# Optimization experiments

Measured on AMD Instinct MI355X. Metric: run time of the kernel, lower is better.

Reference implementation:

```python
import jax, jax.numpy as jnp
import numpy as np

N_NODES = 100000
N_EDGES = 1600000
S_FEAT = 16   # static node features
D_FEAT = 8    # dynamic node features
E_FEAT = 4    # edge features
K = 2
EDGE_IN = E_FEAT + 2 * S_FEAT + 2 * D_FEAT  # 52
HIDDEN = 2 * D_FEAT                          # 16


def setup_inputs() -> dict:
    key = jax.random.key(0)
    ks = jax.random.split(key, 12)
    inp = {
        "x_s": jax.random.normal(ks[0], (N_NODES, S_FEAT), jnp.float32),
        "x_d": jax.random.normal(ks[1], (N_NODES, D_FEAT), jnp.float32),
        "edge_attr": jax.random.normal(ks[2], (N_EDGES, E_FEAT), jnp.float32),
        # edge MLP: Linear(EDGE_IN->HIDDEN) + ReLU + Linear(HIDDEN->D_FEAT)
        "W1": jax.random.normal(ks[3], (HIDDEN, EDGE_IN), jnp.float32) / np.sqrt(EDGE_IN),
        "b1": jnp.zeros((HIDDEN,), jnp.float32),
        "W2": jax.random.normal(ks[4], (D_FEAT, HIDDEN), jnp.float32) / np.sqrt(HIDDEN),
        "b2": jnp.zeros((D_FEAT,), jnp.float32),
        # K+1 = 3 filter matrices, Linear(D->D, bias=False): y = x @ W.T
        "Wf0": jax.random.normal(ks[5], (D_FEAT, D_FEAT), jnp.float32) / np.sqrt(D_FEAT),
        "Wf1": jax.random.normal(ks[6], (D_FEAT, D_FEAT), jnp.float32) / np.sqrt(D_FEAT),
        "Wf2": jax.random.normal(ks[7], (D_FEAT, D_FEAT), jnp.float32) / np.sqrt(D_FEAT),
        "edge_index": jax.random.randint(ks[8], (2, N_EDGES), 0, N_NODES, jnp.int64
                                         if jax.config.jax_enable_x64 else jnp.int32),
    }
    return inp


def _edge_mlp(e, W1, b1, W2, b2):
    h = jax.nn.relu(e @ W1.T + b1)
    return h @ W2.T + b2


def reference(x_s, x_d, edge_attr, W1, b1, W2, b2, Wf0, Wf1, Wf2, edge_index):
    row, col = edge_index[0], edge_index[1]
    num_nodes = x_d.shape[0]

    # s_ij depends only on static inputs (x_s, x_d, edge_attr), not on `out`,
    # so it is identical across the K steps; compute it once. The per-step
    # boolean edge mask is applied multiplicatively below, which matches the
    # torch masked-gather/scatter exactly (normalization is per-edge).
    e_ij = jnp.concatenate(
        [x_s[row], x_s[col], x_d[row], x_d[col], edge_attr], axis=1)  # [E, 52]
    s_ij = _edge_mlp(e_ij, W1, b1, W2, b2)                            # [E, D]
    nrm = jnp.linalg.norm(s_ij, axis=1, keepdims=True)
    s_ij = jnp.where(nrm > 0, s_ij / jnp.where(nrm > 0, nrm, 1.0), 0.0)

    filters = [Wf0, Wf1, Wf2]
    out = x_d @ filters[0].T
    for k in range(K):
        mask = out.sum(1) != 0                         # [N]
        edge_mask = (mask[row] | mask[col]).astype(out.dtype)  # [E]
        hydraulic_gradient = out[col] - out[row]       # [E, D]
        shift_sum = hydraulic_gradient * s_ij * edge_mask[:, None]
        scattered = jax.ops.segment_sum(shift_sum, col, num_segments=num_nodes)
        scattered = scattered @ filters[k + 1].T
        out = out + scattered
    return out
```

## Files before the change

### kernel.cpp

```cpp
#include <hip/hip_runtime.h>
#include <hip/hip_fp16.h>

#define S_FEAT 16
#define D_FEAT 8
#define E_FEAT 4
#define EDGE_IN 52
#define HIDDEN 16
#define SCAN_CHUNK 2048
#define NSUB 8

typedef unsigned int uint4v __attribute__((ext_vector_type(4)));
typedef float float4v __attribute__((ext_vector_type(4)));
typedef int int2v __attribute__((ext_vector_type(2)));

__device__ __forceinline__ void mlp_sij(
    const float* __restrict__ x_s, const float* __restrict__ x_d,
    const float* __restrict__ edge_attr,
    const float* __restrict__ W1, const float* __restrict__ b1,
    const float* __restrict__ W2, const float* __restrict__ b2,
    int row, int col, int e, float s[D_FEAT])
{
    float in[EDGE_IN];
    {
        const float4* p = (const float4*)(x_s + (size_t)row * S_FEAT);
#pragma unroll
        for (int q = 0; q < 4; ++q) {
            float4 v = p[q];
            in[q * 4 + 0] = v.x; in[q * 4 + 1] = v.y;
            in[q * 4 + 2] = v.z; in[q * 4 + 3] = v.w;
        }
    }
    {
        const float4* p = (const float4*)(x_s + (size_t)col * S_FEAT);
#pragma unroll
        for (int q = 0; q < 4; ++q) {
            float4 v = p[q];
            in[16 + q * 4 + 0] = v.x; in[16 + q * 4 + 1] = v.y;
            in[16 + q * 4 + 2] = v.z; in[16 + q * 4 + 3] = v.w;
        }
    }
    {
        const float4* p = (const float4*)(x_d + (size_t)row * D_FEAT);
#pragma unroll
        for (int q = 0; q < 2; ++q) {
            float4 v = p[q];
            in[32 + q * 4 + 0] = v.x; in[32 + q * 4 + 1] = v.y;
            in[32 + q * 4 + 2] = v.z; in[32 + q * 4 + 3] = v.w;
        }
    }
    {
        const float4* p = (const float4*)(x_d + (size_t)col * D_FEAT);
#pragma unroll
        for (int q = 0; q < 2; ++q) {
            float4 v = p[q];
            in[40 + q * 4 + 0] = v.x; in[40 + q * 4 + 1] = v.y;
            in[40 + q * 4 + 2] = v.z; in[40 + q * 4 + 3] = v.w;
        }
    }
    {
        float4 v = *(const float4*)(edge_attr + (size_t)e * E_FEAT);
        in[48] = v.x; in[49] = v.y; in[50] = v.z; in[51] = v.w;
    }

    float h[HIDDEN];
#pragma unroll
    for (int i = 0; i < HIDDEN; ++i) {
        float acc = b1[i];
#pragma unroll
        for (int j = 0; j < EDGE_IN; ++j)
            acc = fmaf(in[j], W1[i * EDGE_IN + j], acc);
        h[i] = acc > 0.f ? acc : 0.f;
    }

    float nrm2 = 0.f;
#pragma unroll
    for (int i = 0; i < D_FEAT; ++i) {
        float acc = b2[i];
#pragma unroll
        for (int j = 0; j < HIDDEN; ++j)
            acc = fmaf(h[j], W2[i * HIDDEN + j], acc);
        s[i] = acc;
        nrm2 = fmaf(acc, acc, nrm2);
    }
    float nrm = sqrtf(nrm2);
    float inv = nrm > 0.f ? 1.f / nrm : 0.f;
#pragma unroll
    for (int i = 0; i < D_FEAT; ++i) s[i] *= inv;
}

__device__ __forceinline__ uint4v pack_rec(const float s[8], int row)
{
    int q[8];
#pragma unroll
    for (int i = 0; i < 8; ++i) {
        float v = fminf(fmaxf(s[i] * 2047.f, -2047.f), 2047.f);
        q[i] = (int)rintf(v) & 0xFFF;
    }
    uint4v r;
    r[0] = (unsigned)(q[0] | (q[1] << 12) | (q[2] << 24));
    r[1] = (unsigned)((q[2] >> 8) | (q[3] << 4) | (q[4] << 16) | (q[5] << 28));
    r[2] = (unsigned)((q[5] >> 4) | (q[6] << 8) | (q[7] << 20));
    r[3] = (unsigned)row;
    return r;
}

__device__ __forceinline__ float rec_s(uint4v r, int f)
{
    int off = f * 12;
    unsigned lo = off < 32 ? r[0] : (off < 64 ? r[1] : r[2]);
    unsigned hi = off < 32 ? r[1] : (off < 64 ? r[2] : 0u);
    unsigned sh = (unsigned)off & 31u;
    unsigned long long both = ((unsigned long long)hi << 32) | lo;
    int q = ((int)((unsigned)(both >> sh) << 20)) >> 20;
    return (float)q * (1.f / 2047.f);
}

__device__ __forceinline__ void unpack8h(uint4v w, float* dst)
{
#pragma unroll
    for (int i = 0; i < 4; ++i) {
        unsigned u = w[i];
        __half2 h = *reinterpret_cast<__half2*>(&u);
        float2 f = __half22float2(h);
        dst[2 * i] = f.x; dst[2 * i + 1] = f.y;
    }
}

__global__ __launch_bounds__(256) void zero_counts_kernel(int* __restrict__ counts, int M)
{
    int i = blockIdx.x * blockDim.x + threadIdx.x;
    if (i < M) counts[i] = 0;
}

__global__ __launch_bounds__(256) void hist_kernel(
    const int* __restrict__ ei, int E, int N, int* __restrict__ counts8)
{
    int e = blockIdx.x * blockDim.x + threadIdx.x;
    if (e >= E) return;
    int col = __builtin_nontemporal_load(ei + E + e);
    atomicAdd(&counts8[(threadIdx.x & (NSUB - 1)) * N + col], 1);
}

__global__ __launch_bounds__(256) void scan_local_kernel(
    const int* __restrict__ counts8, int* __restrict__ partial,
    int* __restrict__ blocksums, int N)
{
    __shared__ int sh[256];
    int b = blockIdx.x, t = threadIdx.x;
    int base = b * SCAN_CHUNK + t * 8;
    int v[8];
    int run = 0;
#pragma unroll
    for (int j = 0; j < 8; ++j) {
        int c = 0;
        if (base + j < N) {
#pragma unroll
            for (int s8 = 0; s8 < NSUB; ++s8)
                c += counts8[s8 * N + base + j];
        }
        v[j] = run;
        run += c;
    }
    sh[t] = run;
    __syncthreads();
#pragma unroll
    for (int st = 1; st < 256; st <<= 1) {
        int x = (t >= st) ? sh[t - st] : 0;
        __syncthreads();
        sh[t] += x;
        __syncthreads();
    }
    int excl = sh[t] - run;
    if (t == 255) blocksums[b] = sh[255];
#pragma unroll
    for (int j = 0; j < 8; ++j)
        if (base + j < N) partial[base + j] = excl + v[j];
}

__global__ __launch_bounds__(64) void scan_blk_kernel(int* __restrict__ bs, int NB)
{
    int lane = threadIdx.x;
    int carry = 0;
    for (int base = 0; base < NB; base += 64) {
        int i = base + lane;
        int orig = (i < NB) ? bs[i] : 0;
        int v = orig;
#pragma unroll
        for (int st = 1; st < 64; st <<= 1) {
            int t = __shfl_up(v, st);
            if (lane >= st) v += t;
        }
        if (i < NB) bs[i] = carry + v - orig;
        carry += __shfl(v, 63);
    }
}

__global__ __launch_bounds__(256) void scan_add_kernel(
    int* __restrict__ offsets, int* __restrict__ cursor,
    const int* __restrict__ blocksums, int N, int E)
{
    int i = blockIdx.x * blockDim.x + threadIdx.x;
    if (i < N) {
        int off = offsets[i] + blocksums[i / SCAN_CHUNK];
        offsets[i] = off;
        cursor[i]  = off;
    } else if (i == N) {
        offsets[N] = E;
    }
}

__global__ __launch_bounds__(256) void proj_scan_kernel(
    int* __restrict__ offsets, int* __restrict__ cursor,
    const int* __restrict__ blocksums,
    const float* __restrict__ x_s, const float* __restrict__ x_d,
    const float* __restrict__ W1, const float* __restrict__ b1,
    const float* __restrict__ Wf0,
    __half* __restrict__ PRh, __half* __restrict__ PCh,
    float* __restrict__ out, int N, int E)
{
    int n = blockIdx.x * blockDim.x + threadIdx.x;
    if (n > N) return;
    if (n == N) { offsets[N] = E; return; }
    {
        int off = offsets[n] + blocksums[n / SCAN_CHUNK];
        offsets[n] = off;
        cursor[n]  = off;
    }
    float xs[S_FEAT], xd[D_FEAT];
    {
        const float4* p = (const float4*)(x_s + (size_t)n * S_FEAT);
#pragma unroll
        for (int q = 0; q < 4; ++q) {
            float4 v = p[q];
            xs[q * 4 + 0] = v.x; xs[q * 4 + 1] = v.y;
            xs[q * 4 + 2] = v.z; xs[q * 4 + 3] = v.w;
        }
        const float4* pd = (const float4*)(x_d + (size_t)n * D_FEAT);
        float4 a = pd[0], b = pd[1];
        xd[0] = a.x; xd[1] = a.y; xd[2] = a.z; xd[3] = a.w;
        xd[4] = b.x; xd[5] = b.y; xd[6] = b.z; xd[7] = b.w;
    }
    __half prh[HIDDEN], pch[HIDDEN];
#pragma unroll
    for (int i = 0; i < HIDDEN; ++i) {
        const float* w = W1 + i * EDGE_IN;
        float a = b1[i], c = 0.f;
#pragma unroll
        for (int j = 0; j < S_FEAT; ++j) {
            a = fmaf(xs[j], w[j], a);
            c = fmaf(xs[j], w[16 + j], c);
        }
#pragma unroll
        for (int j = 0; j < D_FEAT; ++j) {
            a = fmaf(xd[j], w[32 + j], a);
            c = fmaf(xd[j], w[40 + j], c);
        }
        prh[i] = __float2half_rn(a);
        pch[i] = __float2half_rn(c);
    }
    {
        uint4v* pr = (uint4v*)(PRh + (size_t)n * HIDDEN);
        uint4v* pc = (uint4v*)(PCh + (size_t)n * HIDDEN);
        pr[0] = *(uint4v*)&prh[0]; pr[1] = *(uint4v*)&prh[8];
        pc[0] = *(uint4v*)&pch[0]; pc[1] = *(uint4v*)&pch[8];
    }
    float o[D_FEAT];
#pragma unroll
    for (int i = 0; i < D_FEAT; ++i) {
        float acc = 0.f;
#pragma unroll
        for (int j = 0; j < D_FEAT; ++j)
            acc = fmaf(xd[j], Wf0[i * D_FEAT + j], acc);
        o[i] = acc;
    }
    float4* op = (float4*)(out + (size_t)n * D_FEAT);
    op[0] = make_float4(o[0], o[1], o[2], o[3]);
    op[1] = make_float4(o[4], o[5], o[6], o[7]);
}

__device__ __forceinline__ void edge_work(
    const __half* __restrict__ PRh, const __half* __restrict__ PCh,
    const float* __restrict__ edge_attr,
    const float* __restrict__ W1,
    const float* __restrict__ W2, const float* __restrict__ b2,
    int row, int col, int e,
    int* __restrict__ cursor, uint4v* __restrict__ recs)
{
    float pr[HIDDEN], pc[HIDDEN];
    {
        const uint4v* p = (const uint4v*)(PRh + (size_t)row * HIDDEN);
        const uint4v* c = (const uint4v*)(PCh + (size_t)col * HIDDEN);
        uint4v p0 = p[0], p1 = p[1], c0 = c[0], c1 = c[1];
        unpack8h(p0, pr); unpack8h(p1, pr + 8);
        unpack8h(c0, pc); unpack8h(c1, pc + 8);
    }
    float4v ea = __builtin_nontemporal_load(
        (const float4v*)(edge_attr + (size_t)e * E_FEAT));

    float h[HIDDEN];
#pragma unroll
    for (int i = 0; i < HIDDEN; ++i) {
        const float* w = W1 + i * EDGE_IN + 48;
        float acc = pr[i] + pc[i];
        acc = fmaf(ea[0], w[0], acc);
        acc = fmaf(ea[1], w[1], acc);
        acc = fmaf(ea[2], w[2], acc);
        acc = fmaf(ea[3], w[3], acc);
        h[i] = acc > 0.f ? acc : 0.f;
    }

    float s[D_FEAT];
    float nrm2 = 0.f;
#pragma unroll
    for (int i = 0; i < D_FEAT; ++i) {
        float acc = b2[i];
#pragma unroll
        for (int j = 0; j < HIDDEN; ++j)
            acc = fmaf(h[j], W2[i * HIDDEN + j], acc);
        s[i] = acc;
        nrm2 = fmaf(acc, acc, nrm2);
    }
    float nrm = sqrtf(nrm2);
    float inv = nrm > 0.f ? 1.f / nrm : 0.f;
#pragma unroll
    for (int i = 0; i < D_FEAT; ++i) s[i] *= inv;

    uint4v rec = pack_rec(s, row);
    int pos = atomicAdd(&cursor[col], 1);
    __builtin_nontemporal_store(rec, recs + pos);
}

__global__ __launch_bounds__(256) void mlp_scatter_proj_kernel(
    const __half* __restrict__ PRh, const __half* __restrict__ PCh,
    const float* __restrict__ edge_attr,
    const float* __restrict__ W1,
    const float* __restrict__ W2, const float* __restrict__ b2,
    const int* __restrict__ ei, int E,
    int* __restrict__ cursor, uint4v* __restrict__ recs)
{
    int e0 = (blockIdx.x * blockDim.x + threadIdx.x) * 2;
    if (e0 >= E) return;
    if (e0 + 1 < E) {
        int2v rows = __builtin_nontemporal_load((const int2v*)(ei + e0));
        int2v cols = __builtin_nontemporal_load((const int2v*)(ei + E + e0));
        edge_work(PRh, PCh, edge_attr, W1, W2, b2, rows[0], cols[0], e0,     cursor, recs);
        edge_work(PRh, PCh, edge_attr, W1, W2, b2, rows[1], cols[1], e0 + 1, cursor, recs);
    } else {
        int row = ei[e0], col = ei[E + e0];
        edge_work(PRh, PCh, edge_attr, W1, W2, b2, row, col, e0, cursor, recs);
    }
}

__global__ __launch_bounds__(256) void mlp_scatter_direct_kernel(
    const float* __restrict__ x_s, const float* __restrict__ x_d,
    const float* __restrict__ edge_attr,
    const float* __restrict__ W1, const float* __restrict__ b1,
    const float* __restrict__ W2, const float* __restrict__ b2,
    const int* __restrict__ ei, int E,
    int* __restrict__ cursor, uint4v* __restrict__ recs)
{
    int e = blockIdx.x * blockDim.x + threadIdx.x;
    if (e >= E) return;
    int row = ei[e], col = ei[E + e];
    float s[D_FEAT];
    mlp_sij(x_s, x_d, edge_attr, W1, b1, W2, b2, row, col, e, s);
    uint4v rec = pack_rec(s, row);
    int pos = atomicAdd(&cursor[col], 1);
    __builtin_nontemporal_store(rec, recs + pos);
}

__global__ __launch_bounds__(256) void node_init_kernel(
    const float* __restrict__ x_d, const float* __restrict__ Wf0,
    float* __restrict__ out, int N)
{
    int n = blockIdx.x * blockDim.x + threadIdx.x;
    if (n >= N) return;
    float xd[D_FEAT];
    const float4* p = (const float4*)(x_d + (size_t)n * D_FEAT);
    float4 a = p[0], b = p[1];
    xd[0] = a.x; xd[1] = a.y; xd[2] = a.z; xd[3] = a.w;
    xd[4] = b.x; xd[5] = b.y; xd[6] = b.z; xd[7] = b.w;
    float o[D_FEAT];
#pragma unroll
    for (int i = 0; i < D_FEAT; ++i) {
        float acc = 0.f;
#pragma unroll
        for (int j = 0; j < D_FEAT; ++j)
            acc = fmaf(xd[j], Wf0[i * D_FEAT + j], acc);
        o[i] = acc;
    }
    float4* op = (float4*)(out + (size_t)n * D_FEAT);
    op[0] = make_float4(o[0], o[1], o[2], o[3]);
    op[1] = make_float4(o[4], o[5], o[6], o[7]);
}

__global__ __launch_bounds__(256) void csr_step_kernel(
    const float* __restrict__ out_in, float* __restrict__ out_out,
    const int* __restrict__ offsets, const uint4v* __restrict__ recs,
    const float* __restrict__ Wf, int N)
{
    int lane = threadIdx.x & 63;
    int node = blockIdx.x * 4 + (threadIdx.x >> 6);
    if (node >= N) return;
    int e_sub = lane >> 3, f = lane & 7;
    int beg = offsets[node], end = offsets[node + 1];
    float outc = out_in[(size_t)node * 8 + f];
    float sc = outc;
    sc += __shfl_xor(sc, 1); sc += __shfl_xor(sc, 2); sc += __shfl_xor(sc, 4);
    bool mc = (sc != 0.f);
    float acc = 0.f;
    for (int base = beg; base < end; base += 8) {
        int e = base + e_sub;
        bool valid = e < end;
        uint4v rec = (uint4v)(0u);
        if (valid) rec = __builtin_nontemporal_load(recs + e);
        int row = (int)rec[3];
        float s = rec_s(rec, f);
        float outr = out_in[(size_t)row * 8 + f];
        float sr = outr;
        sr += __shfl_xor(sr, 1); sr += __shfl_xor(sr, 2); sr += __shfl_xor(sr, 4);
        acc += (mc || sr != 0.f) ? (outc - outr) * s : 0.f;
    }
    acc += __shfl_xor(acc, 8);
    acc += __shfl_xor(acc, 16);
    acc += __shfl_xor(acc, 32);
    float upd = 0.f;
#pragma unroll
    for (int j = 0; j < 8; ++j) {
        float aj = __shfl(acc, (lane & ~7) | j);
        upd = fmaf(Wf[f * 8 + j], aj, upd);
    }
    if (e_sub == 0)
        out_out[(size_t)node * 8 + f] = outc + upd;
}

__global__ __launch_bounds__(256) void fb_node_init_kernel(
    const float* __restrict__ x_d, const float* __restrict__ Wf0,
    float* __restrict__ out, float* __restrict__ scattered, int N)
{
    int n = blockIdx.x * blockDim.x + threadIdx.x;
    if (n >= N) return;
    float xd[D_FEAT];
    const float4* p = (const float4*)(x_d + (size_t)n * D_FEAT);
    float4 a = p[0], b = p[1];
    xd[0] = a.x; xd[1] = a.y; xd[2] = a.z; xd[3] = a.w;
    xd[4] = b.x; xd[5] = b.y; xd[6] = b.z; xd[7] = b.w;
    float o[D_FEAT];
#pragma unroll
    for (int i = 0; i < D_FEAT; ++i) {
        float acc = 0.f;
#pragma unroll
        for (int j = 0; j < D_FEAT; ++j)
            acc = fmaf(xd[j], Wf0[i * D_FEAT + j], acc);
        o[i] = acc;
    }
    float4* op = (float4*)(out + (size_t)n * D_FEAT);
    op[0] = make_float4(o[0], o[1], o[2], o[3]);
    op[1] = make_float4(o[4], o[5], o[6], o[7]);
    float4* sp = (float4*)(scattered + (size_t)n * D_FEAT);
    sp[0] = make_float4(0.f, 0.f, 0.f, 0.f);
    sp[1] = make_float4(0.f, 0.f, 0.f, 0.f);
}

__global__ __launch_bounds__(256) void fb_edge_step_kernel(
    const float* __restrict__ x_s, const float* __restrict__ x_d,
    const float* __restrict__ edge_attr,
    const float* __restrict__ W1, const float* __restrict__ b1,
    const float* __restrict__ W2, const float* __restrict__ b2,
    const float* __restrict__ out,
    const int* __restrict__ ei, int E, float* __restrict__ scattered)
{
    int e = blockIdx.x * blockDim.x + threadIdx.x;
    if (e >= E) return;
    int row = ei[e], col = ei[E + e];
    const float4* pr = (const float4*)(out + (size_t)row * D_FEAT);
    const float4* pc = (const float4*)(out + (size_t)col * D_FEAT);
    float4 r0 = pr[0], r1 = pr[1], c0 = pc[0], c1 = pc[1];
    float srow = r0.x + r0.y + r0.z + r0.w + r1.x + r1.y + r1.z + r1.w;
    float scol = c0.x + c0.y + c0.z + c0.w + c1.x + c1.y + c1.z + c1.w;
    if (srow == 0.f && scol == 0.f) return;
    float s[D_FEAT];
    mlp_sij(x_s, x_d, edge_attr, W1, b1, W2, b2, row, col, e, s);
    float* dst = scattered + (size_t)col * D_FEAT;
    atomicAdd(dst + 0, (c0.x - r0.x) * s[0]);
    atomicAdd(dst + 1, (c0.y - r0.y) * s[1]);
    atomicAdd(dst + 2, (c0.z - r0.z) * s[2]);
    atomicAdd(dst + 3, (c0.w - r0.w) * s[3]);
    atomicAdd(dst + 4, (c1.x - r1.x) * s[4]);
    atomicAdd(dst + 5, (c1.y - r1.y) * s[5]);
    atomicAdd(dst + 6, (c1.z - r1.z) * s[6]);
    atomicAdd(dst + 7, (c1.w - r1.w) * s[7]);
}

__global__ __launch_bounds__(256) void fb_node_update_kernel(
    float* __restrict__ out, float* __restrict__ scattered,
    const float* __restrict__ Wf, int N)
{
    int n = blockIdx.x * blockDim.x + threadIdx.x;
    if (n >= N) return;
    float sc[D_FEAT];
    float4* sp = (float4*)(scattered + (size_t)n * D_FEAT);
    float4 a = sp[0], b = sp[1];
    sc[0] = a.x; sc[1] = a.y; sc[2] = a.z; sc[3] = a.w;
    sc[4] = b.x; sc[5] = b.y; sc[6] = b.z; sc[7] = b.w;
    sp[0] = make_float4(0.f, 0.f, 0.f, 0.f);
    sp[1] = make_float4(0.f, 0.f, 0.f, 0.f);
    float4* op = (float4*)(out + (size_t)n * D_FEAT);
    float4 o0 = op[0], o1 = op[1];
    float o[D_FEAT] = {o0.x, o0.y, o0.z, o0.w, o1.x, o1.y, o1.z, o1.w};
#pragma unroll
    for (int i = 0; i < D_FEAT; ++i) {
        float acc = 0.f;
#pragma unroll
        for (int j = 0; j < D_FEAT; ++j)
            acc = fmaf(sc[j], Wf[i * D_FEAT + j], acc);
        o[i] += acc;
    }
    op[0] = make_float4(o[0], o[1], o[2], o[3]);
    op[1] = make_float4(o[4], o[5], o[6], o[7]);
}

extern "C" void kernel_launch(void* const* d_in, const int* in_sizes, int n_in,
                              void* d_out, int out_size, void* d_ws, size_t ws_size,
                              hipStream_t stream) {
    const float* x_s       = (const float*)d_in[0];
    const float* x_d       = (const float*)d_in[1];
    const float* edge_attr = (const float*)d_in[2];
    const float* W1        = (const float*)d_in[3];
    const float* b1        = (const float*)d_in[4];
    const float* W2        = (const float*)d_in[5];
    const float* b2        = (const float*)d_in[6];
    const float* Wf[3]     = {(const float*)d_in[7], (const float*)d_in[8],
                              (const float*)d_in[9]};
    const int*   ei        = (const int*)d_in[10];

    const int N = in_sizes[1] / D_FEAT;
    const int E = in_sizes[10] / 2;

    float* out = (float*)d_out;

    size_t off = 0;
    auto carve = [&](size_t bytes) { size_t p = off; off = (off + bytes + 255) & ~255ULL; return p; };
    size_t o_counts  = carve((size_t)NSUB * N * 4);
    size_t o_offsets = carve((size_t)(N + 1) * 4);
    size_t o_cursor  = carve((size_t)(N + 1) * 4);
    size_t o_bsums   = carve(256 * 4);
    size_t o_bufA    = carve((size_t)N * D_FEAT * 4);
    size_t o_recs    = carve((size_t)E * 16);
    const size_t need_base = off;
    size_t o_PR      = carve((size_t)N * HIDDEN * 2);
    size_t o_PC      = carve((size_t)N * HIDDEN * 2);
    const size_t need_full = off;

    dim3 blk(256);
    dim3 gE((E + 255) / 256);
    dim3 gN((N + 255) / 256);

    if (ws_size >= need_base) {
        char* ws = (char*)d_ws;
        int*   counts8 = (int*)(ws + o_counts);
        int*   offsets = (int*)(ws + o_offsets);
        int*   cursor  = (int*)(ws + o_cursor);
        int*   bsums   = (int*)(ws + o_bsums);
        float* bufA    = (float*)(ws + o_bufA);
        uint4v* recs   = (uint4v*)(ws + o_recs);

        const int NB = (N + SCAN_CHUNK - 1) / SCAN_CHUNK;

        zero_counts_kernel<<<dim3((NSUB * N + 255) / 256), blk, 0, stream>>>(counts8, NSUB * N);
        hist_kernel<<<gE, blk, 0, stream>>>(ei, E, N, counts8);
        scan_local_kernel<<<dim3(NB), blk, 0, stream>>>(counts8, offsets, bsums, N);
        scan_blk_kernel<<<dim3(1), dim3(64), 0, stream>>>(bsums, NB);

        if (ws_size >= need_full) {
            __half* PRh = (__half*)(ws + o_PR);
            __half* PCh = (__half*)(ws + o_PC);
            proj_scan_kernel<<<dim3((N + 256) / 256), blk, 0, stream>>>(
                offsets, cursor, bsums, x_s, x_d, W1, b1, Wf[0],
                PRh, PCh, out, N, E);
            mlp_scatter_proj_kernel<<<dim3((E / 2 + 255) / 256), blk, 0, stream>>>(
                PRh, PCh, edge_attr, W1, W2, b2, ei, E, cursor, recs);
        } else {
            scan_add_kernel<<<dim3((N + 256) / 256), blk, 0, stream>>>(offsets, cursor, bsums, N, E);
            node_init_kernel<<<gN, blk, 0, stream>>>(x_d, Wf[0], out, N);
            mlp_scatter_direct_kernel<<<gE, blk, 0, stream>>>(
                x_s, x_d, edge_attr, W1, b1, W2, b2, ei, E, cursor, recs);
        }

        dim3 gC((N + 3) / 4);
        csr_step_kernel<<<gC, blk, 0, stream>>>(out, bufA, offsets, recs, Wf[1], N);
        csr_step_kernel<<<gC, blk, 0, stream>>>(bufA, out, offsets, recs, Wf[2], N);
    } else {
        float* scattered = (float*)d_ws;
        fb_node_init_kernel<<<gN, blk, 0, stream>>>(x_d, Wf[0], out, scattered, N);
        for (int k = 0; k < 2; ++k) {
            fb_edge_step_kernel<<<gE, blk, 0, stream>>>(
                x_s, x_d, edge_attr, W1, b1, W2, b2, out, ei, E, scattered);
            fb_node_update_kernel<<<gN, blk, 0, stream>>>(out, scattered, Wf[k + 1], N);
        }
    }
}
```

Baseline: 375.3 us.

## Fuse all pipeline stages into one cooperative persistent kernel with grid syncs

Replaces the sequence of about eight kernel launches (zero, histogram, scan, block scan, projection, edge MLP scatter, two CSR steps) with a single cooperative kernel of 1024 blocks. The stages are separated by grid.sync() and use grid-stride loops. The aim is to remove per-launch gaps and tail effects between the small kernels. The cost is grid-wide barrier overhead, lower occupancy from the fixed grid size, and the loss of the paired-edge vectorized index loads. If the cooperative launch fails, it falls back to the multi-kernel path.

```diff
diff --git a/kernel.cpp b/kernel.cpp
--- a/kernel.cpp
+++ b/kernel.cpp
@@ -1,5 +1,8 @@
 #include <hip/hip_runtime.h>
 #include <hip/hip_fp16.h>
+#include <hip/hip_cooperative_groups.h>
+
+namespace cg = cooperative_groups;
 
 #define S_FEAT 16
 #define D_FEAT 8
@@ -8,85 +11,10 @@
 #define HIDDEN 16
 #define SCAN_CHUNK 2048
 #define NSUB 8
+#define MEGA_GRID 1024
 
 typedef unsigned int uint4v __attribute__((ext_vector_type(4)));
 typedef float float4v __attribute__((ext_vector_type(4)));
-typedef int int2v __attribute__((ext_vector_type(2)));
-
-__device__ __forceinline__ void mlp_sij(
-    const float* __restrict__ x_s, const float* __restrict__ x_d,
-    const float* __restrict__ edge_attr,
-    const float* __restrict__ W1, const float* __restrict__ b1,
-    const float* __restrict__ W2, const float* __restrict__ b2,
-    int row, int col, int e, float s[D_FEAT])
-{
-    float in[EDGE_IN];
-    {
-        const float4* p = (const float4*)(x_s + (size_t)row * S_FEAT);
-#pragma unroll
-        for (int q = 0; q < 4; ++q) {
-            float4 v = p[q];
-            in[q * 4 + 0] = v.x; in[q * 4 + 1] = v.y;
-            in[q * 4 + 2] = v.z; in[q * 4 + 3] = v.w;
-        }
-    }
-    {
-        const float4* p = (const float4*)(x_s + (size_t)col * S_FEAT);
-#pragma unroll
-        for (int q = 0; q < 4; ++q) {
-            float4 v = p[q];
-            in[16 + q * 4 + 0] = v.x; in[16 + q * 4 + 1] = v.y;
-            in[16 + q * 4 + 2] = v.z; in[16 + q * 4 + 3] = v.w;
-        }
-    }
-    {
-        const float4* p = (const float4*)(x_d + (size_t)row * D_FEAT);
-#pragma unroll
-        for (int q = 0; q < 2; ++q) {
-            float4 v = p[q];
-            in[32 + q * 4 + 0] = v.x; in[32 + q * 4 + 1] = v.y;
-            in[32 + q * 4 + 2] = v.z; in[32 + q * 4 + 3] = v.w;
-        }
-    }
-    {
-        const float4* p = (const float4*)(x_d + (size_t)col * D_FEAT);
-#pragma unroll
-        for (int q = 0; q < 2; ++q) {
-            float4 v = p[q];
-            in[40 + q * 4 + 0] = v.x; in[40 + q * 4 + 1] = v.y;
-            in[40 + q * 4 + 2] = v.z; in[40 + q * 4 + 3] = v.w;
-        }
-    }
-    {
-        float4 v = *(const float4*)(edge_attr + (size_t)e * E_FEAT);
-        in[48] = v.x; in[49] = v.y; in[50] = v.z; in[51] = v.w;
-    }
-
-    float h[HIDDEN];
-#pragma unroll
-    for (int i = 0; i < HIDDEN; ++i) {
-        float acc = b1[i];
-#pragma unroll
-        for (int j = 0; j < EDGE_IN; ++j)
-            acc = fmaf(in[j], W1[i * EDGE_IN + j], acc);
-        h[i] = acc > 0.f ? acc : 0.f;
-    }
-
-    float nrm2 = 0.f;
-#pragma unroll
-    for (int i = 0; i < D_FEAT; ++i) {
-        float acc = b2[i];
-#pragma unroll
-        for (int j = 0; j < HIDDEN; ++j)
-            acc = fmaf(h[j], W2[i * HIDDEN + j], acc);
-        s[i] = acc;
-        nrm2 = fmaf(acc, acc, nrm2);
-    }
-    float nrm = sqrtf(nrm2);
-    float inv = nrm > 0.f ? 1.f / nrm : 0.f;
-#pragma unroll
-    for (int i = 0; i < D_FEAT; ++i) s[i] *= inv;
-}
 
 __device__ __forceinline__ uint4v pack_rec(const float s[8], int row)
 {
@@ -126,6 +54,259 @@
     }
 }
 
+__device__ __forceinline__ void proj_node(
+    int n, const float* __restrict__ x_s, const float* __restrict__ x_d,
+    const float* __restrict__ W1, const float* __restrict__ b1,
+    const float* __restrict__ Wf0,
+    __half* __restrict__ PRh, __half* __restrict__ PCh, float* __restrict__ out)
+{
+    float xs[S_FEAT], xd[D_FEAT];
+    {
+        const float4* p = (const float4*)(x_s + (size_t)n * S_FEAT);
+#pragma unroll
+        for (int q = 0; q < 4; ++q) {
+            float4 v = p[q];
+            xs[q * 4 + 0] = v.x; xs[q * 4 + 1] = v.y;
+            xs[q * 4 + 2] = v.z; xs[q * 4 + 3] = v.w;
+        }
+        const float4* pd = (const float4*)(x_d + (size_t)n * D_FEAT);
+        float4 a = pd[0], b = pd[1];
+        xd[0] = a.x; xd[1] = a.y; xd[2] = a.z; xd[3] = a.w;
+        xd[4] = b.x; xd[5] = b.y; xd[6] = b.z; xd[7] = b.w;
+    }
+    __half prh[HIDDEN], pch[HIDDEN];
+#pragma unroll
+    for (int i = 0; i < HIDDEN; ++i) {
+        const float* w = W1 + i * EDGE_IN;
+        float a = b1[i], c = 0.f;
+#pragma unroll
+        for (int j = 0; j < S_FEAT; ++j) {
+            a = fmaf(xs[j], w[j], a);
+            c = fmaf(xs[j], w[16 + j], c);
+        }
+#pragma unroll
+        for (int j = 0; j < D_FEAT; ++j) {
+            a = fmaf(xd[j], w[32 + j], a);
+            c = fmaf(xd[j], w[40 + j], c);
+        }
+        prh[i] = __float2half_rn(a);
+        pch[i] = __float2half_rn(c);
+    }
+    {
+        uint4v* pr = (uint4v*)(PRh + (size_t)n * HIDDEN);
+        uint4v* pc = (uint4v*)(PCh + (size_t)n * HIDDEN);
+        pr[0] = *(uint4v*)&prh[0]; pr[1] = *(uint4v*)&prh[8];
+        pc[0] = *(uint4v*)&pch[0]; pc[1] = *(uint4v*)&pch[8];
+    }
+    float o[D_FEAT];
+#pragma unroll
+    for (int i = 0; i < D_FEAT; ++i) {
+        float acc = 0.f;
+#pragma unroll
+        for (int j = 0; j < D_FEAT; ++j)
+            acc = fmaf(xd[j], Wf0[i * D_FEAT + j], acc);
+        o[i] = acc;
+    }
+    float4* op = (float4*)(out + (size_t)n * D_FEAT);
+    op[0] = make_float4(o[0], o[1], o[2], o[3]);
+    op[1] = make_float4(o[4], o[5], o[6], o[7]);
+}
+
+__device__ __forceinline__ void edge_work(
+    const __half* __restrict__ PRh, const __half* __restrict__ PCh,
+    const float* __restrict__ edge_attr,
+    const float* __restrict__ W1,
+    const float* __restrict__ W2, const float* __restrict__ b2,
+    int row, int col, int e,
+    int* __restrict__ cursor, uint4v* __restrict__ recs)
+{
+    float pr[HIDDEN], pc[HIDDEN];
+    {
+        const uint4v* p = (const uint4v*)(PRh + (size_t)row * HIDDEN);
+        const uint4v* c = (const uint4v*)(PCh + (size_t)col * HIDDEN);
+        uint4v p0 = p[0], p1 = p[1], c0 = c[0], c1 = c[1];
+        unpack8h(p0, pr); unpack8h(p1, pr + 8);
+        unpack8h(c0, pc); unpack8h(c1, pc + 8);
+    }
+    float4v ea = __builtin_nontemporal_load(
+        (const float4v*)(edge_attr + (size_t)e * E_FEAT));
+
+    float h[HIDDEN];
+#pragma unroll
+    for (int i = 0; i < HIDDEN; ++i) {
+        const float* w = W1 + i * EDGE_IN + 48;
+        float acc = pr[i] + pc[i];
+        acc = fmaf(ea[0], w[0], acc);
+        acc = fmaf(ea[1], w[1], acc);
+        acc = fmaf(ea[2], w[2], acc);
+        acc = fmaf(ea[3], w[3], acc);
+        h[i] = acc > 0.f ? acc : 0.f;
+    }
+
+    float s[D_FEAT];
+    float nrm2 = 0.f;
+#pragma unroll
+    for (int i = 0; i < D_FEAT; ++i) {
+        float acc = b2[i];
+#pragma unroll
+        for (int j = 0; j < HIDDEN; ++j)
+            acc = fmaf(h[j], W2[i * HIDDEN + j], acc);
+        s[i] = acc;
+        nrm2 = fmaf(acc, acc, nrm2);
+    }
+    float nrm = sqrtf(nrm2);
+    float inv = nrm > 0.f ? 1.f / nrm : 0.f;
+#pragma unroll
+    for (int i = 0; i < D_FEAT; ++i) s[i] *= inv;
+
+    uint4v rec = pack_rec(s, row);
+    int pos = atomicAdd(&cursor[col], 1);
+    __builtin_nontemporal_store(rec, recs + pos);
+}
+
+__device__ __forceinline__ void csr_phase(
+    const float* __restrict__ out_in, float* __restrict__ out_out,
+    const int* __restrict__ offsets, const uint4v* __restrict__ recs,
+    const float* __restrict__ Wf, int N)
+{
+    int lane = threadIdx.x & 63;
+    int wid = (blockIdx.x << 2) | (threadIdx.x >> 6);
+    int nwaves = gridDim.x << 2;
+    int e_sub = lane >> 3, f = lane & 7;
+    for (int node = wid; node < N; node += nwaves) {
+        int beg = offsets[node], end = offsets[node + 1];
+        float outc = out_in[(size_t)node * 8 + f];
+        float sc = outc;
+        sc += __shfl_xor(sc, 1); sc += __shfl_xor(sc, 2); sc += __shfl_xor(sc, 4);
+        bool mc = (sc != 0.f);
+        float acc = 0.f;
+        for (int base = beg; base < end; base += 8) {
+            int e = base + e_sub;
+            bool valid = e < end;
+            uint4v rec = (uint4v)(0u);
+            if (valid) rec = __builtin_nontemporal_load(recs + e);
+            int row = (int)rec[3];
+            float s = rec_s(rec, f);
+            float outr = out_in[(size_t)row * 8 + f];
+            float sr = outr;
+            sr += __shfl_xor(sr, 1); sr += __shfl_xor(sr, 2); sr += __shfl_xor(sr, 4);
+            acc += (mc || sr != 0.f) ? (outc - outr) * s : 0.f;
+        }
+        acc += __shfl_xor(acc, 8);
+        acc += __shfl_xor(acc, 16);
+        acc += __shfl_xor(acc, 32);
+        float upd = 0.f;
+#pragma unroll
+        for (int j = 0; j < 8; ++j) {
+            float aj = __shfl(acc, (lane & ~7) | j);
+            upd = fmaf(Wf[f * 8 + j], aj, upd);
+        }
+        if (e_sub == 0)
+            out_out[(size_t)node * 8 + f] = outc + upd;
+    }
+}
+
+__global__ __launch_bounds__(256, 4) void mega_kernel(
+    const int* __restrict__ ei, int E, int N,
+    int* __restrict__ counts8, int* __restrict__ offsets,
+    int* __restrict__ cursor, int* __restrict__ bsums,
+    const float* __restrict__ x_s, const float* __restrict__ x_d,
+    const float* __restrict__ edge_attr,
+    const float* __restrict__ W1, const float* __restrict__ b1,
+    const float* __restrict__ W2, const float* __restrict__ b2,
+    const float* __restrict__ Wf0, const float* __restrict__ Wf1,
+    const float* __restrict__ Wf2,
+    __half* __restrict__ PRh, __half* __restrict__ PCh,
+    float* __restrict__ out, float* __restrict__ bufA,
+    uint4v* __restrict__ recs)
+{
+    cg::grid_group grid = cg::this_grid();
+    const int tid = blockIdx.x * blockDim.x + threadIdx.x;
+    const int nthr = gridDim.x * blockDim.x;
+    const int NB = (N + SCAN_CHUNK - 1) / SCAN_CHUNK;
+    __shared__ int sh[256];
+
+    for (int i = tid; i < NSUB * N; i += nthr) counts8[i] = 0;
+    grid.sync();
+
+    for (int e = tid; e < E; e += nthr) {
+        int col = __builtin_nontemporal_load(ei + E + e);
+        atomicAdd(&counts8[(threadIdx.x & (NSUB - 1)) * N + col], 1);
+    }
+    grid.sync();
+
+    for (int b = blockIdx.x; b < NB; b += gridDim.x) {
+        int t = threadIdx.x;
+        int base = b * SCAN_CHUNK + t * 8;
+        int v[8];
+        int run = 0;
+#pragma unroll
+        for (int j = 0; j < 8; ++j) {
+            int c = 0;
+            if (base + j < N) {
+#pragma unroll
+                for (int s8 = 0; s8 < NSUB; ++s8)
+                    c += counts8[s8 * N + base + j];
+            }
+            v[j] = run;
+            run += c;
+        }
+        sh[t] = run;
+        __syncthreads();
+#pragma unroll
+        for (int st = 1; st < 256; st <<= 1) {
+            int x = (t >= st) ? sh[t - st] : 0;
+            __syncthreads();
+            sh[t] += x;
+            __syncthreads();
+        }
+        int excl = sh[t] - run;
+        if (t == 255) bsums[b] = sh[255];
+#pragma unroll
+        for (int j = 0; j < 8; ++j)
+            if (base + j < N) offsets[base + j] = excl + v[j];
+        __syncthreads();
+    }
+    grid.sync();
+
+    if (blockIdx.x == 0 && threadIdx.x < 64) {
+        int lane = threadIdx.x;
+        int carry = 0;
+        for (int base = 0; base < NB; base += 64) {
+            int i = base + lane;
+            int orig = (i < NB) ? bsums[i] : 0;
+            int v = orig;
+#pragma unroll
+            for (int st = 1; st < 64; st <<= 1) {
+                int t2 = __shfl_up(v, st);
+                if (lane >= st) v += t2;
+            }
+            if (i < NB) bsums[i] = carry + v - orig;
+            carry += __shfl(v, 63);
+        }
+    }
+    grid.sync();
+
+    for (int n = tid; n <= N; n += nthr) {
+        if (n == N) { offsets[N] = E; continue; }
+        int off2 = offsets[n] + bsums[n / SCAN_CHUNK];
+        offsets[n] = off2;
+        cursor[n]  = off2;
+        proj_node(n, x_s, x_d, W1, b1, Wf0, PRh, PCh, out);
+    }
+    grid.sync();
+
+    for (int e = tid; e < E; e += nthr) {
+        int row = ei[e], col = ei[E + e];
+        edge_work(PRh, PCh, edge_attr, W1, W2, b2, row, col, e, cursor, recs);
+    }
+    grid.sync();
+
+    csr_phase(out, bufA, offsets, recs, Wf1, N);
+    grid.sync();
+    csr_phase(bufA, out, offsets, recs, Wf2, N);
+}
+
 __global__ __launch_bounds__(256) void zero_counts_kernel(int* __restrict__ counts, int M)
 {
     int i = blockIdx.x * blockDim.x + threadIdx.x;
@@ -192,20 +373,6 @@
         }
         if (i < NB) bs[i] = carry + v - orig;
         carry += __shfl(v, 63);
-    }
-}
-
-__global__ __launch_bounds__(256) void scan_add_kernel(
-    int* __restrict__ offsets, int* __restrict__ cursor,
-    const int* __restrict__ blocksums, int N, int E)
-{
-    int i = blockIdx.x * blockDim.x + threadIdx.x;
-    if (i < N) {
-        int off = offsets[i] + blocksums[i / SCAN_CHUNK];
-        offsets[i] = off;
-        cursor[i]  = off;
-    } else if (i == N) {
-        offsets[N] = E;
     }
 }
 
@@ -221,113 +388,10 @@
     int n = blockIdx.x * blockDim.x + threadIdx.x;
     if (n > N) return;
     if (n == N) { offsets[N] = E; return; }
-    {
-        int off = offsets[n] + blocksums[n / SCAN_CHUNK];
-        offsets[n] = off;
-        cursor[n]  = off;
-    }
-    float xs[S_FEAT], xd[D_FEAT];
-    {
-        const float4* p = (const float4*)(x_s + (size_t)n * S_FEAT);
-#pragma unroll
-        for (int q = 0; q < 4; ++q) {
-            float4 v = p[q];
-            xs[q * 4 + 0] = v.x; xs[q * 4 + 1] = v.y;
-            xs[q * 4 + 2] = v.z; xs[q * 4 + 3] = v.w;
-        }
-        const float4* pd = (const float4*)(x_d + (size_t)n * D_FEAT);
-        float4 a = pd[0], b = pd[1];
-        xd[0] = a.x; xd[1] = a.y; xd[2] = a.z; xd[3] = a.w;
-        xd[4] = b.x; xd[5] = b.y; xd[6] = b.z; xd[7] = b.w;
-    }
-    __half prh[HIDDEN], pch[HIDDEN];
-#pragma unroll
-    for (int i = 0; i < HIDDEN; ++i) {
-        const float* w = W1 + i * EDGE_IN;
-        float a = b1[i], c = 0.f;
-#pragma unroll
-        for (int j = 0; j < S_FEAT; ++j) {
-            a = fmaf(xs[j], w[j], a);
-            c = fmaf(xs[j], w[16 + j], c);
-        }
-#pragma unroll
-        for (int j = 0; j < D_FEAT; ++j) {
-            a = fmaf(xd[j], w[32 + j], a);
-            c = fmaf(xd[j], w[40 + j], c);
-        }
-        prh[i] = __float2half_rn(a);
-        pch[i] = __float2half_rn(c);
-    }
-    {
-        uint4v* pr = (uint4v*)(PRh + (size_t)n * HIDDEN);
-        uint4v* pc = (uint4v*)(PCh + (size_t)n * HIDDEN);
-        pr[0] = *(uint4v*)&prh[0]; pr[1] = *(uint4v*)&prh[8];
-        pc[0] = *(uint4v*)&pch[0]; pc[1] = *(uint4v*)&pch[8];
-    }
-    float o[D_FEAT];
-#pragma unroll
-    for (int i = 0; i < D_FEAT; ++i) {
-        float acc = 0.f;
-#pragma unroll
-        for (int j = 0; j < D_FEAT; ++j)
-            acc = fmaf(xd[j], Wf0[i * D_FEAT + j], acc);
-        o[i] = acc;
-    }
-    float4* op = (float4*)(out + (size_t)n * D_FEAT);
-    op[0] = make_float4(o[0], o[1], o[2], o[3]);
-    op[1] = make_float4(o[4], o[5], o[6], o[7]);
-}
-
-__device__ __forceinline__ void edge_work(
-    const __half* __restrict__ PRh, const __half* __restrict__ PCh,
-    const float* __restrict__ edge_attr,
-    const float* __restrict__ W1,
-    const float* __restrict__ W2, const float* __restrict__ b2,
-    int row, int col, int e,
-    int* __restrict__ cursor, uint4v* __restrict__ recs)
-{
-    float pr[HIDDEN], pc[HIDDEN];
-    {
-        const uint4v* p = (const uint4v*)(PRh + (size_t)row * HIDDEN);
-        const uint4v* c = (const uint4v*)(PCh + (size_t)col * HIDDEN);
-        uint4v p0 = p[0], p1 = p[1], c0 = c[0], c1 = c[1];
-        unpack8h(p0, pr); unpack8h(p1, pr + 8);
-        unpack8h(c0, pc); unpack8h(c1, pc + 8);
-    }
-    float4v ea = __builtin_nontemporal_load(
-        (const float4v*)(edge_attr + (size_t)e * E_FEAT));
-
-    float h[HIDDEN];
-#pragma unroll
-    for (int i = 0; i < HIDDEN; ++i) {
-        const float* w = W1 + i * EDGE_IN + 48;
-        float acc = pr[i] + pc[i];
-        acc = fmaf(ea[0], w[0], acc);
-        acc = fmaf(ea[1], w[1], acc);
-        acc = fmaf(ea[2], w[2], acc);
-        acc = fmaf(ea[3], w[3], acc);
-        h[i] = acc > 0.f ? acc : 0.f;
-    }
-
-    float s[D_FEAT];
-    float nrm2 = 0.f;
-#pragma unroll
-    for (int i = 0; i < D_FEAT; ++i) {
-        float acc = b2[i];
-#pragma unroll
-        for (int j = 0; j < HIDDEN; ++j)
-            acc = fmaf(h[j], W2[i * HIDDEN + j], acc);
-        s[i] = acc;
-        nrm2 = fmaf(acc, acc, nrm2);
-    }
-    float nrm = sqrtf(nrm2);
-    float inv = nrm > 0.f ? 1.f / nrm : 0.f;
-#pragma unroll
-    for (int i = 0; i < D_FEAT; ++i) s[i] *= inv;
-
-    uint4v rec = pack_rec(s, row);
-    int pos = atomicAdd(&cursor[col], 1);
-    __builtin_nontemporal_store(rec, recs + pos);
+    int off2 = offsets[n] + blocksums[n / SCAN_CHUNK];
+    offsets[n] = off2;
+    cursor[n]  = off2;
+    proj_node(n, x_s, x_d, W1, b1, Wf0, PRh, PCh, out);
 }
 
 __global__ __launch_bounds__(256) void mlp_scatter_proj_kernel(
@@ -338,60 +402,10 @@
     const int* __restrict__ ei, int E,
     int* __restrict__ cursor, uint4v* __restrict__ recs)
 {
-    int e0 = (blockIdx.x * blockDim.x + threadIdx.x) * 2;
-    if (e0 >= E) return;
-    if (e0 + 1 < E) {
-        int2v rows = __builtin_nontemporal_load((const int2v*)(ei + e0));
-        int2v cols = __builtin_nontemporal_load((const int2v*)(ei + E + e0));
-        edge_work(PRh, PCh, edge_attr, W1, W2, b2, rows[0], cols[0], e0,     cursor, recs);
-        edge_work(PRh, PCh, edge_attr, W1, W2, b2, rows[1], cols[1], e0 + 1, cursor, recs);
-    } else {
-        int row = ei[e0], col = ei[E + e0];
-        edge_work(PRh, PCh, edge_attr, W1, W2, b2, row, col, e0, cursor, recs);
-    }
-}
-
-__global__ __launch_bounds__(256) void mlp_scatter_direct_kernel(
-    const float* __restrict__ x_s, const float* __restrict__ x_d,
-    const float* __restrict__ edge_attr,
-    const float* __restrict__ W1, const float* __restrict__ b1,
-    const float* __restrict__ W2, const float* __restrict__ b2,
-    const int* __restrict__ ei, int E,
-    int* __restrict__ cursor, uint4v* __restrict__ recs)
-{
     int e = blockIdx.x * blockDim.x + threadIdx.x;
     if (e >= E) return;
     int row = ei[e], col = ei[E + e];
-    float s[D_FEAT];
-    mlp_sij(x_s, x_d, edge_attr, W1, b1, W2, b2, row, col, e, s);
-    uint4v rec = pack_rec(s, row);
-    int pos = atomicAdd(&cursor[col], 1);
-    __builtin_nontemporal_store(rec, recs + pos);
-}
-
-__global__ __launch_bounds__(256) void node_init_kernel(
-    const float* __restrict__ x_d, const float* __restrict__ Wf0,
-    float* __restrict__ out, int N)
-{
-    int n = blockIdx.x * blockDim.x + threadIdx.x;
-    if (n >= N) return;
-    float xd[D_FEAT];
-    const float4* p = (const float4*)(x_d + (size_t)n * D_FEAT);
-    float4 a = p[0], b = p[1];
-    xd[0] = a.x; xd[1] = a.y; xd[2] = a.z; xd[3] = a.w;
-    xd[4] = b.x; xd[5] = b.y; xd[6] = b.z; xd[7] = b.w;
-    float o[D_FEAT];
-#pragma unroll
-    for (int i = 0; i < D_FEAT; ++i) {
-        float acc = 0.f;
-#pragma unroll
-        for (int j = 0; j < D_FEAT; ++j)
-            acc = fmaf(xd[j], Wf0[i * D_FEAT + j], acc);
-        o[i] = acc;
-    }
-    float4* op = (float4*)(out + (size_t)n * D_FEAT);
-    op[0] = make_float4(o[0], o[1], o[2], o[3]);
-    op[1] = make_float4(o[4], o[5], o[6], o[7]);
+    edge_work(PRh, PCh, edge_attr, W1, W2, b2, row, col, e, cursor, recs);
 }
 
 __global__ __launch_bounds__(256) void csr_step_kernel(
@@ -434,6 +448,136 @@
         out_out[(size_t)node * 8 + f] = outc + upd;
 }
 
+__device__ __forceinline__ void mlp_sij(
+    const float* __restrict__ x_s, const float* __restrict__ x_d,
+    const float* __restrict__ edge_attr,
+    const float* __restrict__ W1, const float* __restrict__ b1,
+    const float* __restrict__ W2, const float* __restrict__ b2,
+    int row, int col, int e, float s[D_FEAT])
+{
+    float in[EDGE_IN];
+    {
+        const float4* p = (const float4*)(x_s + (size_t)row * S_FEAT);
+#pragma unroll
+        for (int q = 0; q < 4; ++q) {
+            float4 v = p[q];
+            in[q * 4 + 0] = v.x; in[q * 4 + 1] = v.y;
+            in[q * 4 + 2] = v.z; in[q * 4 + 3] = v.w;
+        }
+    }
+    {
+        const float4* p = (const float4*)(x_s + (size_t)col * S_FEAT);
+#pragma unroll
+        for (int q = 0; q < 4; ++q) {
+            float4 v = p[q];
+            in[16 + q * 4 + 0] = v.x; in[16 + q * 4 + 1] = v.y;
+            in[16 + q * 4 + 2] = v.z; in[16 + q * 4 + 3] = v.w;
+        }
+    }
+    {
+        const float4* p = (const float4*)(x_d + (size_t)row * D_FEAT);
+#pragma unroll
+        for (int q = 0; q < 2; ++q) {
+            float4 v = p[q];
+            in[32 + q * 4 + 0] = v.x; in[32 + q * 4 + 1] = v.y;
+            in[32 + q * 4 + 2] = v.z; in[32 + q * 4 + 3] = v.w;
+        }
+    }
+    {
+        const float4* p = (const float4*)(x_d + (size_t)col * D_FEAT);
+#pragma unroll
+        for (int q = 0; q < 2; ++q) {
+            float4 v = p[q];
+            in[40 + q * 4 + 0] = v.x; in[40 + q * 4 + 1] = v.y;
+            in[40 + q * 4 + 2] = v.z; in[40 + q * 4 + 3] = v.w;
+        }
+    }
+    {
+        float4 v = *(const float4*)(edge_attr + (size_t)e * E_FEAT);
+        in[48] = v.x; in[49] = v.y; in[50] = v.z; in[51] = v.w;
+    }
+    float h[HIDDEN];
+#pragma unroll
+    for (int i = 0; i < HIDDEN; ++i) {
+        float acc = b1[i];
+#pragma unroll
+        for (int j = 0; j < EDGE_IN; ++j)
+            acc = fmaf(in[j], W1[i * EDGE_IN + j], acc);
+        h[i] = acc > 0.f ? acc : 0.f;
+    }
+    float nrm2 = 0.f;
+#pragma unroll
+    for (int i = 0; i < D_FEAT; ++i) {
+        float acc = b2[i];
+#pragma unroll
+        for (int j = 0; j < HIDDEN; ++j)
+            acc = fmaf(h[j], W2[i * HIDDEN + j], acc);
+        s[i] = acc;
+        nrm2 = fmaf(acc, acc, nrm2);
+    }
+    float nrm = sqrtf(nrm2);
+    float inv = nrm > 0.f ? 1.f / nrm : 0.f;
+#pragma unroll
+    for (int i = 0; i < D_FEAT; ++i) s[i] *= inv;
+}
+
+__global__ __launch_bounds__(256) void mlp_scatter_direct_kernel(
+    const float* __restrict__ x_s, const float* __restrict__ x_d,
+    const float* __restrict__ edge_attr,
+    const float* __restrict__ W1, const float* __restrict__ b1,
+    const float* __restrict__ W2, const float* __restrict__ b2,
+    const int* __restrict__ ei, int E,
+    int* __restrict__ cursor, uint4v* __restrict__ recs)
+{
+    int e = blockIdx.x * blockDim.x + threadIdx.x;
+    if (e >= E) return;
+    int row = ei[e], col = ei[E + e];
+    float s[D_FEAT];
+    mlp_sij(x_s, x_d, edge_attr, W1, b1, W2, b2, row, col, e, s);
+    uint4v rec = pack_rec(s, row);
+    int pos = atomicAdd(&cursor[col], 1);
+    __builtin_nontemporal_store(rec, recs + pos);
+}
+
+__global__ __launch_bounds__(256) void scan_add_kernel(
+    int* __restrict__ offsets, int* __restrict__ cursor,
+    const int* __restrict__ blocksums, int N, int E)
+{
+    int i = blockIdx.x * blockDim.x + threadIdx.x;
+    if (i < N) {
+        int off2 = offsets[i] + blocksums[i / SCAN_CHUNK];
+        offsets[i] = off2;
+        cursor[i]  = off2;
+    } else if (i == N) {
+        offsets[N] = E;
+    }
+}
+
+__global__ __launch_bounds__(256) void node_init_kernel(
+    const float* __restrict__ x_d, const float* __restrict__ Wf0,
+    float* __restrict__ out, int N)
+{
+    int n = blockIdx.x * blockDim.x + threadIdx.x;
+    if (n >= N) return;
+    float xd[D_FEAT];
+    const float4* p = (const float4*)(x_d + (size_t)n * D_FEAT);
+    float4 a = p[0], b = p[1];
+    xd[0] = a.x; xd[1] = a.y; xd[2] = a.z; xd[3] = a.w;
+    xd[4] = b.x; xd[5] = b.y; xd[6] = b.z; xd[7] = b.w;
+    float o[D_FEAT];
+#pragma unroll
+    for (int i = 0; i < D_FEAT; ++i) {
+        float acc = 0.f;
+#pragma unroll
+        for (int j = 0; j < D_FEAT; ++j)
+            acc = fmaf(xd[j], Wf0[i * D_FEAT + j], acc);
+        o[i] = acc;
+    }
+    float4* op = (float4*)(out + (size_t)n * D_FEAT);
+    op[0] = make_float4(o[0], o[1], o[2], o[3]);
+    op[1] = make_float4(o[4], o[5], o[6], o[7]);
+}
+
 __global__ __launch_bounds__(256) void fb_node_init_kernel(
     const float* __restrict__ x_d, const float* __restrict__ Wf0,
     float* __restrict__ out, float* __restrict__ scattered, int N)
@@ -530,12 +674,13 @@
     const float* b1        = (const float*)d_in[4];
     const float* W2        = (const float*)d_in[5];
     const float* b2        = (const float*)d_in[6];
-    const float* Wf[3]     = {(const float*)d_in[7], (const float*)d_in[8],
-                              (const float*)d_in[9]};
+    const float* Wf0       = (const float*)d_in[7];
+    const float* Wf1       = (const float*)d_in[8];
+    const float* Wf2       = (const float*)d_in[9];
     const int*   ei        = (const int*)d_in[10];
 
-    const int N = in_sizes[1] / D_FEAT;
-    const int E = in_sizes[10] / 2;
+    int N = in_sizes[1] / D_FEAT;
+    int E = in_sizes[10] / 2;
 
     float* out = (float*)d_out;
 
@@ -567,36 +712,55 @@
 
         const int NB = (N + SCAN_CHUNK - 1) / SCAN_CHUNK;
 
-        zero_counts_kernel<<<dim3((NSUB * N + 255) / 256), blk, 0, stream>>>(counts8, NSUB * N);
-        hist_kernel<<<gE, blk, 0, stream>>>(ei, E, N, counts8);
-        scan_local_kernel<<<dim3(NB), blk, 0, stream>>>(counts8, offsets, bsums, N);
-        scan_blk_kernel<<<dim3(1), dim3(64), 0, stream>>>(bsums, NB);
-
         if (ws_size >= need_full) {
             __half* PRh = (__half*)(ws + o_PR);
             __half* PCh = (__half*)(ws + o_PC);
+
+            void* args[] = {
+                (void*)&ei, (void*)&E, (void*)&N,
+                (void*)&counts8, (void*)&offsets, (void*)&cursor, (void*)&bsums,
+                (void*)&x_s, (void*)&x_d, (void*)&edge_attr,
+                (void*)&W1, (void*)&b1, (void*)&W2, (void*)&b2,
+                (void*)&Wf0, (void*)&Wf1, (void*)&Wf2,
+                (void*)&PRh, (void*)&PCh,
+                (void*)&out, (void*)&bufA, (void*)&recs
+            };
+            hipError_t cerr = hipLaunchCooperativeKernel(
+                (const void*)mega_kernel, dim3(MEGA_GRID), blk, args, 0, stream);
+            if (cerr == hipSuccess) return;
+
+            zero_counts_kernel<<<dim3((NSUB * N + 255) / 256), blk, 0, stream>>>(counts8, NSUB * N);
+            hist_kernel<<<gE, blk, 0, stream>>>(ei, E, N, counts8);
+            scan_local_kernel<<<dim3(NB), blk, 0, stream>>>(counts8, offsets, bsums, N);
+            scan_blk_kernel<<<dim3(1), dim3(64), 0, stream>>>(bsums, NB);
             proj_scan_kernel<<<dim3((N + 256) / 256), blk, 0, stream>>>(
-                offsets, cursor, bsums, x_s, x_d, W1, b1, Wf[0],
-                PRh, PCh, out, N, E);
-            mlp_scatter_proj_kernel<<<dim3((E / 2 + 255) / 256), blk, 0, stream>>>(
+                offsets, cursor, bsums, x_s, x_d, W1, b1, Wf0, PRh, PCh, out, N, E);
+            mlp_scatter_proj_kernel<<<gE, blk, 0, stream>>>(
                 PRh, PCh, edge_attr, W1, W2, b2, ei, E, cursor, recs);
+            dim3 gC((N + 3) / 4);
+            csr_step_kernel<<<gC, blk, 0, stream>>>(out, bufA, offsets, recs, Wf1, N);
+            csr_step_kernel<<<gC, blk, 0, stream>>>(bufA, out, offsets, recs, Wf2, N);
         } else {
+            zero_counts_kernel<<<dim3((NSUB * N + 255) / 256), blk, 0, stream>>>(counts8, NSUB * N);
+            hist_kernel<<<gE, blk, 0, stream>>>(ei, E, N, counts8);
+            scan_local_kernel<<<dim3(NB), blk, 0, stream>>>(counts8, offsets, bsums, N);
+            scan_blk_kernel<<<dim3(1), dim3(64), 0, stream>>>(bsums, NB);
             scan_add_kernel<<<dim3((N + 256) / 256), blk, 0, stream>>>(offsets, cursor, bsums, N, E);
-            node_init_kernel<<<gN, blk, 0, stream>>>(x_d, Wf[0], out, N);
+            node_init_kernel<<<gN, blk, 0, stream>>>(x_d, Wf0, out, N);
             mlp_scatter_direct_kernel<<<gE, blk, 0, stream>>>(
                 x_s, x_d, edge_attr, W1, b1, W2, b2, ei, E, cursor, recs);
-        }
-
-        dim3 gC((N + 3) / 4);
-        csr_step_kernel<<<gC, blk, 0, stream>>>(out, bufA, offsets, recs, Wf[1], N);
-        csr_step_kernel<<<gC, blk, 0, stream>>>(bufA, out, offsets, recs, Wf[2], N);
+            dim3 gC((N + 3) / 4);
+            csr_step_kernel<<<gC, blk, 0, stream>>>(out, bufA, offsets, recs, Wf1, N);
+            csr_step_kernel<<<gC, blk, 0, stream>>>(bufA, out, offsets, recs, Wf2, N);
+        }
     } else {
         float* scattered = (float*)d_ws;
-        fb_node_init_kernel<<<gN, blk, 0, stream>>>(x_d, Wf[0], out, scattered, N);
+        fb_node_init_kernel<<<gN, blk, 0, stream>>>(x_d, Wf0, out, scattered, N);
         for (int k = 0; k < 2; ++k) {
+            const float* Wfk = (k == 0) ? Wf1 : Wf2;
             fb_edge_step_kernel<<<gE, blk, 0, stream>>>(
                 x_s, x_d, edge_attr, W1, b1, W2, b2, out, ei, E, scattered);
-            fb_node_update_kernel<<<gN, blk, 0, stream>>>(out, scattered, Wf[k + 1], N);
-        }
-    }
-}
+            fb_node_update_kernel<<<gN, blk, 0, stream>>>(out, scattered, Wfk, N);
+        }
+    }
+}
```

Result: slower. 1.234 ms (+228.8%).
